# Kernel optimization log

Measured on AMD Instinct MI355X. Metric: run time of the kernel, lower is better.

The kernel has to match this reference:

```python
import jax, jax.numpy as jnp
import numpy as np

B, C, H, W = 8, 256, 64, 64
CQK = C // 8  # 32


def setup_inputs() -> dict:
    key = jax.random.key(0)
    ks = jax.random.split(key, 8)
    s = 0.05
    return {
        "x": jax.random.normal(ks[0], (B, C, H, W), dtype=jnp.float32),
        "wq": jax.random.normal(ks[1], (CQK, C), dtype=jnp.float32) * s,
        "bq": jax.random.normal(ks[2], (CQK,), dtype=jnp.float32) * s,
        "wk": jax.random.normal(ks[3], (CQK, C), dtype=jnp.float32) * s,
        "bk": jax.random.normal(ks[4], (CQK,), dtype=jnp.float32) * s,
        "wv": jax.random.normal(ks[5], (C, C), dtype=jnp.float32) * s,
        "bv": jax.random.normal(ks[6], (C,), dtype=jnp.float32) * s,
        "gamma": jax.random.normal(ks[7], (1,), dtype=jnp.float32),
    }


def reference(x, wq, bq, wk, bk, wv, bv, gamma):
    b, c, h, w = x.shape
    xf = x.reshape(b, c, h * w)  # [B, C, N]
    # conv1d kernel-size-1 == per-token linear over channels
    f = jnp.einsum('oc,bcn->bon', wq, xf) + bq[None, :, None]  # [B, C/8, N]
    g = jnp.einsum('oc,bcn->bon', wk, xf) + bk[None, :, None]  # [B, C/8, N]
    hh = jnp.einsum('oc,bcn->bon', wv, xf) + bv[None, :, None]  # [B, C, N]
    # scores[b, i, j] = sum_o f[b, o, i] * g[b, o, j]; NO 1/sqrt(d) scaling
    scores = jnp.einsum('boi,boj->bij', f, g)  # [B, N, N]
    # softmax over dim=1 (the f/query index axis), as in the original
    beta = jax.nn.softmax(scores, axis=1)
    # o[b, c, j] = gamma * sum_i hh[b, c, i] * beta[b, i, j] + xf
    o = gamma[0] * jnp.einsum('bci,bij->bcj', hh, beta) + xf
    return o.reshape(b, c, h, w)
```

## Files before the change

kernel.cpp:

```cpp
#include <hip/hip_runtime.h>

#define B_ 8
#define C_ 256
#define N_ 4096
#define LOG2E 1.44269504088896f
#define SHIFT 14.0f

typedef _Float16 half8 __attribute__((ext_vector_type(8)));
typedef _Float16 half4 __attribute__((ext_vector_type(4)));
typedef float floatx4 __attribute__((ext_vector_type(4)));

__global__ __launch_bounds__(256) void k_transpose(const float* __restrict__ x,
                                                   _Float16* __restrict__ xT) {
    __shared__ float tile[64][65];
    int i0 = blockIdx.x * 64;
    int c0 = blockIdx.y * 64;
    int b  = blockIdx.z;
    int t   = threadIdx.x;
    int col = t & 63;
    int rb  = t >> 6;
    const float* xb = x + ((size_t)(b * C_ + c0)) * N_ + i0;
#pragma unroll
    for (int k = 0; k < 16; ++k) {
        int r = rb * 16 + k;
        tile[r][col] = xb[(size_t)r * N_ + col];
    }
    __syncthreads();
    _Float16* xTb = xT + ((size_t)(b * N_ + i0)) * C_ + c0;
#pragma unroll
    for (int k = 0; k < 16; ++k) {
        int r2 = rb * 16 + k;
        xTb[(size_t)r2 * C_ + col] = (_Float16)tile[col][r2];
    }
}

__global__ __launch_bounds__(256) void k_wprep(const float* __restrict__ wq, const float* __restrict__ bq,
                                               const float* __restrict__ wk, const float* __restrict__ bk,
                                               const float* __restrict__ wv, const float* __restrict__ bv,
                                               _Float16* __restrict__ Wh, float* __restrict__ Bh) {
    int r = blockIdx.x;
    int t = threadIdx.x;
    const float* src;
    float bias;
    if (r < 32)      { src = wq + r * 256;        bias = bq[r]; }
    else if (r < 64) { src = wk + (r - 32) * 256; bias = bk[r - 32]; }
    else             { src = wv + (r - 64) * 256; bias = bv[r - 64]; }
    Wh[r * 256 + t] = (_Float16)src[t];
    if (t == 0) Bh[r] = bias;
}

__global__ __launch_bounds__(256, 2) void k_proj(const _Float16* __restrict__ xT,
                                                 const _Float16* __restrict__ Wh,
                                                 const float* __restrict__ Bh,
                                                 _Float16* __restrict__ FG,
                                                 _Float16* __restrict__ V) {
    __shared__ _Float16 As[64 * 40] __attribute__((aligned(16)));
    __shared__ _Float16 Bs[320 * 40] __attribute__((aligned(16)));
    int id = blockIdx.x;
    int b  = id & 7;
    int i0 = (id >> 3) * 64;
    int t = threadIdx.x;
    int w = t >> 6, lane = t & 63, col = lane & 15, q = lane >> 4;
    floatx4 acc[4][5];
#pragma unroll
    for (int mt = 0; mt < 4; ++mt)
#pragma unroll
        for (int nt = 0; nt < 5; ++nt) acc[mt][nt] = (floatx4){0.f, 0.f, 0.f, 0.f};
    const _Float16* xTb = xT + ((size_t)(b * N_ + i0)) * 256;
    for (int kc = 0; kc < 8; ++kc) {
        int k0 = kc * 32;
        {
            int i = t >> 2, part = t & 3;
            *(uint4*)&As[i * 40 + part * 8] = *(const uint4*)&xTb[(size_t)i * 256 + k0 + part * 8];
        }
#pragma unroll
        for (int rep = 0; rep < 5; ++rep) {
            int idx = t + rep * 256;
            int row = idx >> 2, part = idx & 3;
            *(uint4*)&Bs[row * 40 + part * 8] = *(const uint4*)&Wh[row * 256 + k0 + part * 8];
        }
        __syncthreads();
        half8 a[4], bf[5];
#pragma unroll
        for (int mt = 0; mt < 4; ++mt) a[mt] = *(const half8*)&As[(mt * 16 + col) * 40 + q * 8];
#pragma unroll
        for (int nt = 0; nt < 5; ++nt) bf[nt] = *(const half8*)&Bs[(w * 80 + nt * 16 + col) * 40 + q * 8];
#pragma unroll
        for (int mt = 0; mt < 4; ++mt)
#pragma unroll
            for (int nt = 0; nt < 5; ++nt)
                acc[mt][nt] = __builtin_amdgcn_mfma_f32_16x16x32_f16(a[mt], bf[nt], acc[mt][nt], 0, 0, 0);
        __syncthreads();
    }
#pragma unroll
    for (int nt = 0; nt < 5; ++nt) {
        int n = w * 80 + nt * 16 + col;
        float bias = Bh[n];
        if (n < 64) {
#pragma unroll
            for (int mt = 0; mt < 4; ++mt)
#pragma unroll
                for (int r = 0; r < 4; ++r) {
                    int i = i0 + mt * 16 + q * 4 + r;
                    FG[((size_t)(b * N_ + i)) * 64 + n] = (_Float16)(acc[mt][nt][r] + bias);
                }
        } else {
            int c = n - 64;
            _Float16* Vp = V + ((size_t)(b * C_ + c)) * N_ + i0;
#pragma unroll
            for (int mt = 0; mt < 4; ++mt) {
                half4 v4;
#pragma unroll
                for (int r = 0; r < 4; ++r) v4[r] = (_Float16)(acc[mt][nt][r] + bias);
                *(half4*)&Vp[mt * 16 + q * 4] = v4;
            }
        }
    }
}

__global__ __launch_bounds__(256, 2) void k_attn(const _Float16* __restrict__ FG,
                                                 const _Float16* __restrict__ V,
                                                 const float* __restrict__ x,
                                                 const float* __restrict__ gptr,
                                                 float* __restrict__ out) {
    __shared__ _Float16 Qs[64 * 40] __attribute__((aligned(16)));
    __shared__ _Float16 Ks[64 * 40] __attribute__((aligned(16)));
    __shared__ _Float16 Vs[256 * 88] __attribute__((aligned(16)));
    __shared__ _Float16 Ps[64 * 72] __attribute__((aligned(16)));
    __shared__ float linv[64];
    int id = blockIdx.x;
    int b  = id & 7;
    int j0 = (id >> 3) * 64;
    int t = threadIdx.x;
    int w = t >> 6, lane = t & 63, col = lane & 15, q = lane >> 4;
    const _Float16* FGb = FG + ((size_t)b * N_) * 64;
    const _Float16* Vb  = V + ((size_t)(b * C_)) * N_;
    {
        int j = t >> 2, part = t & 3;
        *(uint4*)&Qs[j * 40 + part * 8] = *(const uint4*)&FGb[(size_t)(j0 + j) * 64 + 32 + part * 8];
    }
    floatx4 acc[4][4];
#pragma unroll
    for (int ct = 0; ct < 4; ++ct)
#pragma unroll
        for (int jt = 0; jt < 4; ++jt) acc[ct][jt] = (floatx4){0.f, 0.f, 0.f, 0.f};
    float lacc = 0.f;
    __syncthreads();
    half8 bq = *(const half8*)&Qs[(w * 16 + col) * 40 + q * 8];
    for (int it = 0; it < 64; ++it) {
        int i0 = it * 64;
        {
            int i = t >> 2, part = t & 3;
            *(uint4*)&Ks[i * 40 + part * 8] = *(const uint4*)&FGb[(size_t)(i0 + i) * 64 + part * 8];
        }
#pragma unroll
        for (int rep = 0; rep < 8; ++rep) {
            int idx = t + rep * 256;
            int c = idx >> 3, part = idx & 7;
            *(uint4*)&Vs[c * 88 + part * 8] = *(const uint4*)&Vb[(size_t)c * N_ + i0 + part * 8];
        }
        __syncthreads();
#pragma unroll
        for (int itile = 0; itile < 4; ++itile) {
            half8 a = *(const half8*)&Ks[(itile * 16 + col) * 40 + q * 8];
            floatx4 s = __builtin_amdgcn_mfma_f32_16x16x32_f16(a, bq, (floatx4){0.f, 0.f, 0.f, 0.f}, 0, 0, 0);
            half4 ph;
#pragma unroll
            for (int r = 0; r < 4; ++r) {
                float p = exp2f((s[r] - SHIFT) * LOG2E);
                lacc += p;
                ph[r] = (_Float16)p;
            }
            *(half4*)&Ps[(w * 16 + col) * 72 + itile * 16 + q * 4] = ph;
        }
        __syncthreads();
#pragma unroll
        for (int kk = 0; kk < 2; ++kk) {
            half8 bfr[4], afr[4];
#pragma unroll
            for (int jt = 0; jt < 4; ++jt)
                bfr[jt] = *(const half8*)&Ps[(jt * 16 + col) * 72 + kk * 32 + q * 8];
#pragma unroll
            for (int ct = 0; ct < 4; ++ct)
                afr[ct] = *(const half8*)&Vs[(w * 64 + ct * 16 + col) * 88 + kk * 32 + q * 8];
#pragma unroll
            for (int ct = 0; ct < 4; ++ct)
#pragma unroll
                for (int jt = 0; jt < 4; ++jt)
                    acc[ct][jt] = __builtin_amdgcn_mfma_f32_16x16x32_f16(afr[ct], bfr[jt], acc[ct][jt], 0, 0, 0);
        }
        __syncthreads();
    }
    lacc += __shfl_xor(lacc, 16, 64);
    lacc += __shfl_xor(lacc, 32, 64);
    if (lane < 16) linv[w * 16 + lane] = 1.0f / lacc;
    __syncthreads();
    float gamma = gptr[0];
    const float* xb = x + ((size_t)(b * C_)) * N_;
    float* ob = out + ((size_t)(b * C_)) * N_;
#pragma unroll
    for (int jt = 0; jt < 4; ++jt) {
        float li = linv[jt * 16 + col];
        int j = j0 + jt * 16 + col;
#pragma unroll
        for (int ct = 0; ct < 4; ++ct)
#pragma unroll
            for (int r = 0; r < 4; ++r) {
                int c = w * 64 + ct * 16 + q * 4 + r;
                size_t off = (size_t)c * N_ + j;
                ob[off] = gamma * acc[ct][jt][r] * li + xb[off];
            }
    }
}

extern "C" void kernel_launch(void* const* d_in, const int* in_sizes, int n_in,
                              void* d_out, int out_size, void* d_ws, size_t ws_size,
                              hipStream_t stream) {
    const float* x  = (const float*)d_in[0];
    const float* wq = (const float*)d_in[1];
    const float* bq = (const float*)d_in[2];
    const float* wk = (const float*)d_in[3];
    const float* bk = (const float*)d_in[4];
    const float* wv = (const float*)d_in[5];
    const float* bv = (const float*)d_in[6];
    const float* gm = (const float*)d_in[7];
    float* out = (float*)d_out;
    char* ws = (char*)d_ws;
    _Float16* xT = (_Float16*)ws;
    _Float16* FG = (_Float16*)(ws + 16777216);
    _Float16* V  = (_Float16*)(ws + 20971520);
    _Float16* Wh = (_Float16*)(ws + 37748736);
    float*    Bh = (float*)(ws + 37912576);

    k_transpose<<<dim3(64, 4, 8), 256, 0, stream>>>(x, xT);
    k_wprep<<<dim3(320), 256, 0, stream>>>(wq, bq, wk, bk, wv, bv, Wh, Bh);
    k_proj<<<dim3(512), 256, 0, stream>>>(xT, Wh, Bh, FG, V);
    k_attn<<<dim3(512), 256, 0, stream>>>(FG, V, x, gm, out);
}
```

Before: 223.8 us.

## Load V and K fragments directly from global and double-buffer P in attention kernel

The attention kernel now uses 512-thread blocks covering 128 query columns. Each wave loads its V and K MFMA fragments straight from global memory into registers instead of staging them in shared memory. The P tile is double-buffered, which removes one of the two barriers per iteration. The transpose kernel also switches to vectorized float4 loads and half8 stores. The aim is to cut LDS traffic and synchronization, at the cost of uncoalesced strided global reads of V and doubling the number of K fetches across blocks.

```diff
diff --git a/kernel.cpp b/kernel.cpp
--- a/kernel.cpp
+++ b/kernel.cpp
@@ -16,21 +16,25 @@
     int i0 = blockIdx.x * 64;
     int c0 = blockIdx.y * 64;
     int b  = blockIdx.z;
-    int t   = threadIdx.x;
-    int col = t & 63;
-    int rb  = t >> 6;
+    int t  = threadIdx.x;
     const float* xb = x + ((size_t)(b * C_ + c0)) * N_ + i0;
-#pragma unroll
-    for (int k = 0; k < 16; ++k) {
-        int r = rb * 16 + k;
-        tile[r][col] = xb[(size_t)r * N_ + col];
+    int r4 = t >> 4;
+    int c4 = (t & 15) * 4;
+#pragma unroll
+    for (int k = 0; k < 4; ++k) {
+        int r = k * 16 + r4;
+        *(float4*)&tile[r][c4] = *(const float4*)&xb[(size_t)r * N_ + c4];
     }
     __syncthreads();
     _Float16* xTb = xT + ((size_t)(b * N_ + i0)) * C_ + c0;
-#pragma unroll
-    for (int k = 0; k < 16; ++k) {
-        int r2 = rb * 16 + k;
-        xTb[(size_t)r2 * C_ + col] = (_Float16)tile[col][r2];
+    int i2 = t >> 2;
+#pragma unroll
+    for (int g = 0; g < 2; ++g) {
+        int ch = (t & 3) + g * 4;
+        half8 v;
+#pragma unroll
+        for (int j = 0; j < 8; ++j) v[j] = (_Float16)tile[ch * 8 + j][i2];
+        *(half8*)&xTb[(size_t)i2 * C_ + ch * 8] = v;
     }
 }
 
@@ -118,52 +122,46 @@
     }
 }
 
-__global__ __launch_bounds__(256, 2) void k_attn(const _Float16* __restrict__ FG,
+__global__ __launch_bounds__(512, 2) void k_attn(const _Float16* __restrict__ FG,
                                                  const _Float16* __restrict__ V,
                                                  const float* __restrict__ x,
                                                  const float* __restrict__ gptr,
                                                  float* __restrict__ out) {
-    __shared__ _Float16 Qs[64 * 40] __attribute__((aligned(16)));
-    __shared__ _Float16 Ks[64 * 40] __attribute__((aligned(16)));
-    __shared__ _Float16 Vs[256 * 88] __attribute__((aligned(16)));
-    __shared__ _Float16 Ps[64 * 72] __attribute__((aligned(16)));
-    __shared__ float linv[64];
+    __shared__ _Float16 Ps[2][128 * 72] __attribute__((aligned(16)));
+    __shared__ float linv[128];
     int id = blockIdx.x;
     int b  = id & 7;
-    int j0 = (id >> 3) * 64;
+    int j0 = (id >> 3) * 128;
     int t = threadIdx.x;
     int w = t >> 6, lane = t & 63, col = lane & 15, q = lane >> 4;
-    const _Float16* FGb = FG + ((size_t)b * N_) * 64;
-    const _Float16* Vb  = V + ((size_t)(b * C_)) * N_;
-    {
-        int j = t >> 2, part = t & 3;
-        *(uint4*)&Qs[j * 40 + part * 8] = *(const uint4*)&FGb[(size_t)(j0 + j) * 64 + 32 + part * 8];
-    }
+    int cb = (w & 3) * 64;
+    int jh = (w >> 2) * 64;
+    const _Float16* FGb = FG + (size_t)b * N_ * 64;
+    const _Float16* Vb  = V + (size_t)b * C_ * N_;
+    half8 bq = *(const half8*)&FGb[(size_t)(j0 + w * 16 + col) * 64 + 32 + q * 8];
     floatx4 acc[4][4];
 #pragma unroll
     for (int ct = 0; ct < 4; ++ct)
 #pragma unroll
         for (int jt = 0; jt < 4; ++jt) acc[ct][jt] = (floatx4){0.f, 0.f, 0.f, 0.f};
     float lacc = 0.f;
-    __syncthreads();
-    half8 bq = *(const half8*)&Qs[(w * 16 + col) * 40 + q * 8];
     for (int it = 0; it < 64; ++it) {
         int i0 = it * 64;
-        {
-            int i = t >> 2, part = t & 3;
-            *(uint4*)&Ks[i * 40 + part * 8] = *(const uint4*)&FGb[(size_t)(i0 + i) * 64 + part * 8];
-        }
-#pragma unroll
-        for (int rep = 0; rep < 8; ++rep) {
-            int idx = t + rep * 256;
-            int c = idx >> 3, part = idx & 7;
-            *(uint4*)&Vs[c * 88 + part * 8] = *(const uint4*)&Vb[(size_t)c * N_ + i0 + part * 8];
-        }
-        __syncthreads();
+        half8 afr[2][4];
+#pragma unroll
+        for (int kk = 0; kk < 2; ++kk)
+#pragma unroll
+            for (int ct = 0; ct < 4; ++ct)
+                afr[kk][ct] = *(const half8*)&Vb[(size_t)(cb + ct * 16 + col) * N_ + i0 + kk * 32 + q * 8];
+        half8 aK[4];
+#pragma unroll
+        for (int itile = 0; itile < 4; ++itile)
+            aK[itile] = *(const half8*)&FGb[(size_t)(i0 + itile * 16 + col) * 64 + q * 8];
+        _Float16* Pw = Ps[it & 1];
 #pragma unroll
         for (int itile = 0; itile < 4; ++itile) {
-            half8 a = *(const half8*)&Ks[(itile * 16 + col) * 40 + q * 8];
-            floatx4 s = __builtin_amdgcn_mfma_f32_16x16x32_f16(a, bq, (floatx4){0.f, 0.f, 0.f, 0.f}, 0, 0, 0);
+            floatx4 s = __builtin_amdgcn_mfma_f32_16x16x32_f16(aK[itile], bq,
+                                                               (floatx4){0.f, 0.f, 0.f, 0.f}, 0, 0, 0);
             half4 ph;
 #pragma unroll
             for (int r = 0; r < 4; ++r) {
@@ -171,25 +169,21 @@
                 lacc += p;
                 ph[r] = (_Float16)p;
             }
-            *(half4*)&Ps[(w * 16 + col) * 72 + itile * 16 + q * 4] = ph;
+            *(half4*)&Pw[(w * 16 + col) * 72 + itile * 16 + q * 4] = ph;
         }
         __syncthreads();
 #pragma unroll
         for (int kk = 0; kk < 2; ++kk) {
-            half8 bfr[4], afr[4];
+            half8 bfr[4];
 #pragma unroll
             for (int jt = 0; jt < 4; ++jt)
-                bfr[jt] = *(const half8*)&Ps[(jt * 16 + col) * 72 + kk * 32 + q * 8];
+                bfr[jt] = *(const half8*)&Pw[(jh + jt * 16 + col) * 72 + kk * 32 + q * 8];
 #pragma unroll
             for (int ct = 0; ct < 4; ++ct)
-                afr[ct] = *(const half8*)&Vs[(w * 64 + ct * 16 + col) * 88 + kk * 32 + q * 8];
-#pragma unroll
-            for (int ct = 0; ct < 4; ++ct)
 #pragma unroll
                 for (int jt = 0; jt < 4; ++jt)
-                    acc[ct][jt] = __builtin_amdgcn_mfma_f32_16x16x32_f16(afr[ct], bfr[jt], acc[ct][jt], 0, 0, 0);
-        }
-        __syncthreads();
+                    acc[ct][jt] = __builtin_amdgcn_mfma_f32_16x16x32_f16(afr[kk][ct], bfr[jt], acc[ct][jt], 0, 0, 0);
+        }
     }
     lacc += __shfl_xor(lacc, 16, 64);
     lacc += __shfl_xor(lacc, 32, 64);
@@ -200,13 +194,13 @@
     float* ob = out + ((size_t)(b * C_)) * N_;
 #pragma unroll
     for (int jt = 0; jt < 4; ++jt) {
-        float li = linv[jt * 16 + col];
-        int j = j0 + jt * 16 + col;
+        float li = linv[jh + jt * 16 + col];
+        int j = j0 + jh + jt * 16 + col;
 #pragma unroll
         for (int ct = 0; ct < 4; ++ct)
 #pragma unroll
             for (int r = 0; r < 4; ++r) {
-                int c = w * 64 + ct * 16 + q * 4 + r;
+                int c = cb + ct * 16 + q * 4 + r;
                 size_t off = (size_t)c * N_ + j;
                 ob[off] = gamma * acc[ct][jt][r] * li + xb[off];
             }
@@ -235,5 +229,5 @@
     k_transpose<<<dim3(64, 4, 8), 256, 0, stream>>>(x, xT);
     k_wprep<<<dim3(320), 256, 0, stream>>>(wq, bq, wk, bk, wv, bv, Wh, Bh);
     k_proj<<<dim3(512), 256, 0, stream>>>(xT, Wh, Bh, FG, V);
-    k_attn<<<dim3(512), 256, 0, stream>>>(FG, V, x, gm, out);
-}
+    k_attn<<<dim3(256), 512, 0, stream>>>(FG, V, x, gm, out);
+}
```

Measured after the change: 348.8 us. +55.8%, slower.
